# Performance work log

Hardware: AMD Instinct MI355X
Metric: run time of the kernel (lower is better)

Reference implementation:

```python
import jax, jax.numpy as jnp
import numpy as np

B, N, H, D2 = 2, 2048, 16, 64


def setup_inputs() -> dict:
    key = jax.random.key(0)
    k1, k2, k3 = jax.random.split(key, 3)
    keys = jax.random.normal(k1, (B, N, H, D2), dtype=jnp.float32)
    queries = jax.random.normal(k2, (B, N, H, D2), dtype=jnp.float32)
    values = jax.random.normal(k3, (B, N, H, D2), dtype=jnp.float32)
    return {"keys": keys, "queries": queries, "values": values}


def reference(keys, queries, values):
    b, n, h, d2 = keys.shape
    # Faithful to the original: torch uses .reshape (NOT transpose) to go
    # (b, n, h, d2) -> (b, h, n, d2), a pure memory reinterpretation.
    q = queries.reshape(b, h, n, d2)
    k = keys.reshape(b, h, n, d2)
    v = values.reshape(b, h, n, d2)
    scale = 1.0 / (d2 ** 0.5)
    # [b, h, n, n] attention scores
    scores = jnp.einsum('bhqd,bhkd->bhqk', q, k) * scale
    # causal mask: upper triangle (diagonal=1) set to -inf
    causal = jnp.triu(jnp.ones((n, n), dtype=bool), k=1)
    scores = jnp.where(causal, -jnp.inf, scores)
    attn = jax.nn.softmax(scores, axis=-1)
    out = jnp.einsum('bhqk,bhkd->bhqd', attn, v)
    return out.reshape(b, n, h, d2)
```

## Files before the change

### kernel.cpp

```cpp
#include <hip/hip_runtime.h>


typedef short  short4v __attribute__((ext_vector_type(4)));
typedef short  short8v __attribute__((ext_vector_type(8)));
typedef float  float4v __attribute__((ext_vector_type(4)));
typedef float  float8v __attribute__((ext_vector_type(8)));

#define NQ 2048
#define DD 64
#define KT 64
#define KP 72
#define VP 72

union U2 { unsigned int u[2]; short4v s; };
union U4 { unsigned int u[4]; short8v s; };

static __device__ __forceinline__ unsigned int pktr(float lo, float hi) {
    return __builtin_amdgcn_perm(__builtin_bit_cast(unsigned int, hi),
                                 __builtin_bit_cast(unsigned int, lo),
                                 0x07060302);
}
static __device__ __forceinline__ unsigned int pkrn(float lo, float hi) {
    unsigned int a = __builtin_bit_cast(unsigned int, hi) + 0x8000u;
    unsigned int b = __builtin_bit_cast(unsigned int, lo) + 0x8000u;
    return __builtin_amdgcn_perm(a, b, 0x07060302);
}

__global__ __launch_bounds__(512, 4) void mha_fwd_kernel(
    const float* __restrict__ Kg,
    const float* __restrict__ Qg,
    const float* __restrict__ Vg,
    float* __restrict__ Og)
{
    __shared__ __align__(16) unsigned short Klds[2][KT * KP];
    __shared__ __align__(16) unsigned short Vt[2][DD * VP];

    const int t    = threadIdx.x;
    const int lane = t & 63;
    const int wave = t >> 6;
    const int col  = lane & 15;
    const int quad = lane >> 4;

    const int b  = blockIdx.x;
    const int bh = (b & 7) * 4 + ((b >> 3) & 3);
    const int h  = b >> 5;
    const int p  = (h < 8) ? h : 23 - h;

    const int T    = (wave < 4) ? (31 - p) : p;
    const int q0   = T * 64 + (wave & 3) * 16;
    const int qg   = q0 + col;
    const int kmax = T * 64;
    const int nt   = 32 - p;

    const size_t base = (size_t)bh * NQ * DD;
    const float* Qp = Qg + base;
    const float* Kp = Kg + base;
    const float* Vp = Vg + base;
    float*       Op = Og + base;

    const float sscale = 0.125f * 1.4426950408889634f;

    const int kr = t >> 3, kc = (t & 7) * 8;
    const int vd = t & 63, vg = (t >> 6) * 8;
    const int kvb = (wave & 1) * 32 + (wave >> 1) * 4;

    short8v qf0, qf1;
    {
        float8v a = *(const float8v*)(Qp + (size_t)qg * DD + quad * 8);
        float8v c = *(const float8v*)(Qp + (size_t)qg * DD + 32 + quad * 8);
        U4 w0, w1;
#pragma unroll
        for (int i = 0; i < 4; ++i) {
            w0.u[i] = pkrn(a[2 * i] * sscale, a[2 * i + 1] * sscale);
            w1.u[i] = pkrn(c[2 * i] * sscale, c[2 * i + 1] * sscale);
        }
        qf0 = w0.s;
        qf1 = w1.s;
    }

    float l_i = 0.0f;
    float4v o[4];
#pragma unroll
    for (int d = 0; d < 4; ++d) o[d] = (float4v){0.f, 0.f, 0.f, 0.f};

    {
        float8v ka = *(const float8v*)(Kp + (size_t)kr * DD + kc);
        float vr[8];
#pragma unroll
        for (int i = 0; i < 8; ++i)
            vr[i] = Vp[(size_t)(kvb + (i >> 2) * 16 + (i & 3)) * DD + vd];
        U4 wk, wv;
#pragma unroll
        for (int i = 0; i < 4; ++i) {
            wk.u[i] = pktr(ka[2 * i], ka[2 * i + 1]);
            wv.u[i] = pktr(vr[2 * i], vr[2 * i + 1]);
        }
        *(short8v*)&Klds[0][kr * KP + kc] = wk.s;
        *(short8v*)&Vt[0][vd * VP + vg]   = wv.s;
    }
    __syncthreads();

    for (int it = 0; it < nt; ++it) {
        const int cur   = it & 1;
        const int kb    = it * KT;
        const bool stage = (it + 1 < nt);

        float8v ka;
        float vr[8];
        if (stage) {
            const int nkb = kb + KT;
            ka = *(const float8v*)(Kp + (size_t)(nkb + kr) * DD + kc);
#pragma unroll
            for (int i = 0; i < 8; ++i)
                vr[i] = Vp[(size_t)(nkb + kvb + (i >> 2) * 16 + (i & 3)) * DD + vd];
        }

        if (kb <= kmax) {
            __builtin_amdgcn_s_setprio(1);

            float4v sT[4];
#pragma unroll
            for (int u = 0; u < 4; ++u) {
                short8v kf0 = *(const short8v*)&Klds[cur][(u * 16 + col) * KP + quad * 8];
                short8v kf1 = *(const short8v*)&Klds[cur][(u * 16 + col) * KP + 32 + quad * 8];
                sT[u] = (float4v){0.f, 0.f, 0.f, 0.f};
                sT[u] = __builtin_amdgcn_mfma_f32_16x16x32_bf16(kf0, qf0, sT[u], 0, 0, 0);
                sT[u] = __builtin_amdgcn_mfma_f32_16x16x32_bf16(kf1, qf1, sT[u], 0, 0, 0);
            }

            if (kb == kmax) {
#pragma unroll
                for (int u = 0; u < 4; ++u)
#pragma unroll
                    for (int r = 0; r < 4; ++r) {
                        const int key = kb + u * 16 + quad * 4 + r;
                        if (key > qg) sT[u][r] = -3.0e38f;
                    }
            }

            short4v pf[4];
#pragma unroll
            for (int u = 0; u < 4; ++u) {
#pragma unroll
                for (int r = 0; r < 4; ++r) {
                    sT[u][r] = exp2f(sT[u][r]);
                    l_i += sT[u][r];
                }
                U2 w;
                w.u[0] = pktr(sT[u][0], sT[u][1]);
                w.u[1] = pktr(sT[u][2], sT[u][3]);
                pf[u] = w.s;
            }

#pragma unroll
            for (int d = 0; d < 4; ++d) {
                short8v v01 = *(const short8v*)&Vt[cur][(d * 16 + col) * VP + quad * 16];
                short8v v23 = *(const short8v*)&Vt[cur][(d * 16 + col) * VP + quad * 16 + 8];
                short4v f0 = __builtin_shufflevector(v01, v01, 0, 1, 2, 3);
                short4v f1 = __builtin_shufflevector(v01, v01, 4, 5, 6, 7);
                short4v f2 = __builtin_shufflevector(v23, v23, 0, 1, 2, 3);
                short4v f3 = __builtin_shufflevector(v23, v23, 4, 5, 6, 7);
                o[d] = __builtin_amdgcn_mfma_f32_16x16x16bf16_1k(pf[0], f0, o[d], 0, 0, 0);
                o[d] = __builtin_amdgcn_mfma_f32_16x16x16bf16_1k(pf[1], f1, o[d], 0, 0, 0);
                o[d] = __builtin_amdgcn_mfma_f32_16x16x16bf16_1k(pf[2], f2, o[d], 0, 0, 0);
                o[d] = __builtin_amdgcn_mfma_f32_16x16x16bf16_1k(pf[3], f3, o[d], 0, 0, 0);
            }

            __builtin_amdgcn_s_setprio(0);
        }

        if (stage) {
            U4 wk, wv;
#pragma unroll
            for (int i = 0; i < 4; ++i) {
                wk.u[i] = pktr(ka[2 * i], ka[2 * i + 1]);
                wv.u[i] = pktr(vr[2 * i], vr[2 * i + 1]);
            }
            *(short8v*)&Klds[cur ^ 1][kr * KP + kc] = wk.s;
            *(short8v*)&Vt[cur ^ 1][vd * VP + vg]   = wv.s;
        }

        __syncthreads();
    }

    float rs = l_i;
    rs += __shfl_xor(rs, 16);
    rs += __shfl_xor(rs, 32);
    float lv[4];
#pragma unroll
    for (int r = 0; r < 4; ++r) lv[r] = 1.0f / __shfl(rs, quad * 4 + r, 64);
#pragma unroll
    for (int r = 0; r < 4; ++r)
#pragma unroll
        for (int d = 0; d < 4; ++d)
            Op[(size_t)(q0 + quad * 4 + r) * DD + d * 16 + col] = o[d][r] * lv[r];
}

extern "C" void kernel_launch(void* const* d_in, const int* in_sizes, int n_in,
                              void* d_out, int out_size, void* d_ws, size_t ws_size,
                              hipStream_t stream) {
    const float* keys    = (const float*)d_in[0];
    const float* queries = (const float*)d_in[1];
    const float* values  = (const float*)d_in[2];
    float* out           = (float*)d_out;

    dim3 grid(2 * 16 * 16);
    dim3 block(512, 1, 1);
    mha_fwd_kernel<<<grid, block, 0, stream>>>(keys, queries, values, out);
}
```

Before: 120.7 us.

## Split paired-tile blocks into single-tile 256-thread blocks with heavy-first ordering

Each 512-thread block used to pair a long and a short causal query tile, so both halves walked the longer key range. Blocks are now 256 threads, each owning one 64-row query tile, with 1024 blocks ordered longest-first. Each thread now stages twice as much K/V into LDS. This removes the iterations where the short tile's waves sat idle behind the long tile, at the cost of more blocks and more staging work per thread.

```diff
diff --git a/kernel.cpp b/kernel.cpp
--- a/kernel.cpp
+++ b/kernel.cpp
@@ -26,7 +26,7 @@
     return __builtin_amdgcn_perm(a, b, 0x07060302);
 }
 
-__global__ __launch_bounds__(512, 4) void mha_fwd_kernel(
+__global__ __launch_bounds__(256, 4) void mha_fwd_kernel(
     const float* __restrict__ Kg,
     const float* __restrict__ Qg,
     const float* __restrict__ Vg,
@@ -41,16 +41,19 @@
     const int col  = lane & 15;
     const int quad = lane >> 4;
 
-    const int b  = blockIdx.x;
-    const int bh = (b & 7) * 4 + ((b >> 3) & 3);
-    const int h  = b >> 5;
-    const int p  = (h < 8) ? h : 23 - h;
-
-    const int T    = (wave < 4) ? (31 - p) : p;
-    const int q0   = T * 64 + (wave & 3) * 16;
+    const int b   = blockIdx.x;
+    const int r   = b & 255;
+    const int qtr = b >> 8;
+    const int bh  = r & 31;
+    const int j   = r >> 5;
+    const int T   = (qtr == 0) ? (31 - j)
+                  : (qtr == 1) ? (16 + j)
+                  : (qtr == 2) ? (15 - j) : j;
+
+    const int nt   = T + 1;
+    const int q0   = T * 64 + wave * 16;
     const int qg   = q0 + col;
     const int kmax = T * 64;
-    const int nt   = 32 - p;
 
     const size_t base = (size_t)bh * NQ * DD;
     const float* Qp = Qg + base;
@@ -61,8 +64,8 @@
     const float sscale = 0.125f * 1.4426950408889634f;
 
     const int kr = t >> 3, kc = (t & 7) * 8;
-    const int vd = t & 63, vg = (t >> 6) * 8;
-    const int kvb = (wave & 1) * 32 + (wave >> 1) * 4;
+    const int vd = t & 63, vg = (t >> 6) * 16;
+    const int kvb = (t >> 6) * 4;
 
     short8v qf0, qf1;
     {
@@ -83,39 +86,45 @@
 #pragma unroll
     for (int d = 0; d < 4; ++d) o[d] = (float4v){0.f, 0.f, 0.f, 0.f};
 
+    float8v ka0, ka1;
+    float   vr[16];
+
     {
-        float8v ka = *(const float8v*)(Kp + (size_t)kr * DD + kc);
-        float vr[8];
-#pragma unroll
-        for (int i = 0; i < 8; ++i)
+        ka0 = *(const float8v*)(Kp + (size_t)kr * DD + kc);
+        ka1 = *(const float8v*)(Kp + (size_t)(kr + 32) * DD + kc);
+#pragma unroll
+        for (int i = 0; i < 16; ++i)
             vr[i] = Vp[(size_t)(kvb + (i >> 2) * 16 + (i & 3)) * DD + vd];
-        U4 wk, wv;
+        U4 w0, w1, wv0, wv1;
 #pragma unroll
         for (int i = 0; i < 4; ++i) {
-            wk.u[i] = pktr(ka[2 * i], ka[2 * i + 1]);
-            wv.u[i] = pktr(vr[2 * i], vr[2 * i + 1]);
-        }
-        *(short8v*)&Klds[0][kr * KP + kc] = wk.s;
-        *(short8v*)&Vt[0][vd * VP + vg]   = wv.s;
+            w0.u[i]  = pktr(ka0[2 * i], ka0[2 * i + 1]);
+            w1.u[i]  = pktr(ka1[2 * i], ka1[2 * i + 1]);
+            wv0.u[i] = pktr(vr[2 * i], vr[2 * i + 1]);
+            wv1.u[i] = pktr(vr[8 + 2 * i], vr[9 + 2 * i]);
+        }
+        *(short8v*)&Klds[0][kr * KP + kc]        = w0.s;
+        *(short8v*)&Klds[0][(kr + 32) * KP + kc] = w1.s;
+        *(short8v*)&Vt[0][vd * VP + vg]          = wv0.s;
+        *(short8v*)&Vt[0][vd * VP + vg + 8]      = wv1.s;
     }
     __syncthreads();
 
     for (int it = 0; it < nt; ++it) {
-        const int cur   = it & 1;
-        const int kb    = it * KT;
+        const int cur = it & 1;
+        const int kb  = it * KT;
         const bool stage = (it + 1 < nt);
 
-        float8v ka;
-        float vr[8];
         if (stage) {
             const int nkb = kb + KT;
-            ka = *(const float8v*)(Kp + (size_t)(nkb + kr) * DD + kc);
-#pragma unroll
-            for (int i = 0; i < 8; ++i)
+            ka0 = *(const float8v*)(Kp + (size_t)(nkb + kr) * DD + kc);
+            ka1 = *(const float8v*)(Kp + (size_t)(nkb + kr + 32) * DD + kc);
+#pragma unroll
+            for (int i = 0; i < 16; ++i)
                 vr[i] = Vp[(size_t)(nkb + kvb + (i >> 2) * 16 + (i & 3)) * DD + vd];
         }
 
-        if (kb <= kmax) {
+        {
             __builtin_amdgcn_s_setprio(1);
 
             float4v sT[4];
@@ -132,9 +141,9 @@
 #pragma unroll
                 for (int u = 0; u < 4; ++u)
 #pragma unroll
-                    for (int r = 0; r < 4; ++r) {
-                        const int key = kb + u * 16 + quad * 4 + r;
-                        if (key > qg) sT[u][r] = -3.0e38f;
+                    for (int rr = 0; rr < 4; ++rr) {
+                        const int key = kb + u * 16 + quad * 4 + rr;
+                        if (key > qg) sT[u][rr] = -3.0e38f;
                     }
             }
 
@@ -142,9 +151,9 @@
 #pragma unroll
             for (int u = 0; u < 4; ++u) {
 #pragma unroll
-                for (int r = 0; r < 4; ++r) {
-                    sT[u][r] = exp2f(sT[u][r]);
-                    l_i += sT[u][r];
+                for (int rr = 0; rr < 4; ++rr) {
+                    sT[u][rr] = exp2f(sT[u][rr]);
+                    l_i += sT[u][rr];
                 }
                 U2 w;
                 w.u[0] = pktr(sT[u][0], sT[u][1]);
@@ -170,14 +179,18 @@
         }
 
         if (stage) {
-            U4 wk, wv;
+            U4 w0, w1, wv0, wv1;
 #pragma unroll
             for (int i = 0; i < 4; ++i) {
-                wk.u[i] = pktr(ka[2 * i], ka[2 * i + 1]);
-                wv.u[i] = pktr(vr[2 * i], vr[2 * i + 1]);
-            }
-            *(short8v*)&Klds[cur ^ 1][kr * KP + kc] = wk.s;
-            *(short8v*)&Vt[cur ^ 1][vd * VP + vg]   = wv.s;
+                w0.u[i]  = pktr(ka0[2 * i], ka0[2 * i + 1]);
+                w1.u[i]  = pktr(ka1[2 * i], ka1[2 * i + 1]);
+                wv0.u[i] = pktr(vr[2 * i], vr[2 * i + 1]);
+                wv1.u[i] = pktr(vr[8 + 2 * i], vr[9 + 2 * i]);
+            }
+            *(short8v*)&Klds[cur ^ 1][kr * KP + kc]        = w0.s;
+            *(short8v*)&Klds[cur ^ 1][(kr + 32) * KP + kc] = w1.s;
+            *(short8v*)&Vt[cur ^ 1][vd * VP + vg]          = wv0.s;
+            *(short8v*)&Vt[cur ^ 1][vd * VP + vg + 8]      = wv1.s;
         }
 
         __syncthreads();
@@ -188,12 +201,12 @@
     rs += __shfl_xor(rs, 32);
     float lv[4];
 #pragma unroll
-    for (int r = 0; r < 4; ++r) lv[r] = 1.0f / __shfl(rs, quad * 4 + r, 64);
-#pragma unroll
-    for (int r = 0; r < 4; ++r)
+    for (int rr = 0; rr < 4; ++rr) lv[rr] = 1.0f / __shfl(rs, quad * 4 + rr, 64);
+#pragma unroll
+    for (int rr = 0; rr < 4; ++rr)
 #pragma unroll
         for (int d = 0; d < 4; ++d)
-            Op[(size_t)(q0 + quad * 4 + r) * DD + d * 16 + col] = o[d][r] * lv[r];
+            Op[(size_t)(q0 + quad * 4 + rr) * DD + d * 16 + col] = o[d][rr] * lv[rr];
 }
 
 extern "C" void kernel_launch(void* const* d_in, const int* in_sizes, int n_in,
@@ -204,7 +217,7 @@
     const float* values  = (const float*)d_in[2];
     float* out           = (float*)d_out;
 
-    dim3 grid(2 * 16 * 16);
-    dim3 block(512, 1, 1);
+    dim3 grid(1024);
+    dim3 block(256, 1, 1);
     mha_fwd_kernel<<<grid, block, 0, stream>>>(keys, queries, values, out);
 }
```

After: 126.0 us. +4.4%, slower.
